# Optimization experiments

Measured on AMD Instinct MI355X. Metric: run time of the kernel, lower is better.

The kernel has to match this reference:

```python
import jax, jax.numpy as jnp
import numpy as np

N, E, F, H, G, C = 50000, 800000, 768, 256, 512, 2  # H = nhid*2 (nhid=128), G graphs, C classes
NHID = 128


def setup_inputs() -> dict:
    key = jax.random.key(0)
    ks = jax.random.split(key, 18)
    s = 0.05
    x = jax.random.normal(ks[0], (N, F), jnp.float32)
    edge_index = jax.random.randint(ks[1], (2, E), 0, N, dtype=jnp.int32)
    # sorted batch vector; every graph non-empty so the 'first node per graph' gather is valid
    batch = ((jnp.arange(N) * G) // N).astype(jnp.int32)
    return {
        "x": x,
        "edge_index": edge_index,
        "batch": batch,
        # GATConv 1 (in=F, out=H, heads=1)
        "W1": jax.random.normal(ks[2], (F, H), jnp.float32) * s,
        "as1": jax.random.normal(ks[3], (H,), jnp.float32) * s,
        "ad1": jax.random.normal(ks[4], (H,), jnp.float32) * s,
        "b1": jnp.zeros((H,), jnp.float32),
        # GATConv 2 (in=H, out=H)
        "W2": jax.random.normal(ks[5], (H, H), jnp.float32) * s,
        "as2": jax.random.normal(ks[6], (H,), jnp.float32) * s,
        "ad2": jax.random.normal(ks[7], (H,), jnp.float32) * s,
        "b2": jnp.zeros((H,), jnp.float32),
        # fc0: num_features -> nhid (news branch)
        "W0": jax.random.normal(ks[8], (F, NHID), jnp.float32) * s,
        "b0": jnp.zeros((NHID,), jnp.float32),
        # fc1: 2*nhid -> nhid (used twice, as in the source)
        "Wf1": jax.random.normal(ks[9], (H, NHID), jnp.float32) * s,
        "bf1": jnp.zeros((NHID,), jnp.float32),
        # fc2: nhid -> num_classes
        "Wf2": jax.random.normal(ks[10], (NHID, C), jnp.float32) * s,
        "bf2": jnp.zeros((C,), jnp.float32),
    }


def _gat(x, src, dst, W, a_s, a_d, b):
    # PyG GATConv, heads=1, concat=True, negative_slope=0.2, self-loops pre-appended to src/dst.
    h = x @ W                                   # [N, H]
    e = jax.nn.leaky_relu((h @ a_s)[src] + (h @ a_d)[dst], 0.2)  # [E+N]
    m = jax.ops.segment_max(e, dst, num_segments=N)
    ex = jnp.exp(e - m[dst])                    # stable segment softmax numerator
    denom = jax.ops.segment_sum(ex, dst, num_segments=N)
    agg = jax.ops.segment_sum(ex[:, None] * h[src], dst, num_segments=N)  # [N, H]
    return agg / denom[:, None] + b


def reference(x, edge_index, batch, W1, as1, ad1, b1, W2, as2, ad2, b2, W0, b0, Wf1, bf1, Wf2, bf2):
    loop = jnp.arange(N, dtype=edge_index.dtype)
    src = jnp.concatenate([edge_index[0], loop])  # add self-loops (PyG default)
    dst = jnp.concatenate([edge_index[1], loop])
    h = jax.nn.selu(_gat(x, src, dst, W1, as1, ad1, b1))
    h = jax.nn.selu(_gat(h, src, dst, W2, as2, ad2, b2))
    # global mean pool over graphs
    cnt = jax.ops.segment_sum(jnp.ones((N,), h.dtype), batch, num_segments=G)
    pooled = jax.nn.selu(jax.ops.segment_sum(h, batch, num_segments=G) / cnt[:, None])
    z = jax.nn.selu(pooled @ Wf1 + bf1)
    # dropout(p=0.5) in eval mode -> identity
    # concat branch: first node of each graph (news root)
    first_idx = jax.ops.segment_min(jnp.arange(N), batch, num_segments=G)
    news = jax.nn.relu(x[first_idx] @ W0 + b0)
    z = jnp.concatenate([z, news], axis=1)       # [G, 2*nhid]
    z = jax.nn.relu(z @ Wf1 + bf1)
    return jax.nn.log_softmax(z @ Wf2 + bf2, axis=-1)
```

## Files before the change

kernel.cpp:

```cpp
#include <hip/hip_runtime.h>
#include <hip/hip_bf16.h>
#include <cstdint>
#include <cstddef>

#define NN 50000
#define EE 800000
#define FF 768
#define HH 256
#define GG 512
#define CC 2
#define NHIDD 128
#define ETOT (EE + NN)
#define NCHUNK 49

typedef __attribute__((ext_vector_type(8))) short bf16x8;
typedef __attribute__((ext_vector_type(4))) float f32x4;
typedef __attribute__((ext_vector_type(8))) unsigned short us8;

__device__ __forceinline__ float b2f(unsigned short u){
  union { float f; uint32_t i; } v; v.i = ((uint32_t)u) << 16; return v.f;
}
__device__ __forceinline__ unsigned short f2b(float f){
  uint32_t u = __float_as_uint(f);
  uint32_t r = (u + 0x7fffu + ((u >> 16) & 1u)) >> 16;
  return (unsigned short)r;
}
__device__ __forceinline__ uint32_t cvtpk(float a, float b){
  uint32_t d;
  asm volatile("v_cvt_pk_bf16_f32 %0, %1, %2" : "=v"(d) : "v"(a), "v"(b));
  return d;
}
__device__ __forceinline__ float selu_f(float x){
  const float lam = 1.0507009873554805f, alp = 1.6732632423543772f;
  return x > 0.f ? lam * x : lam * alp * (__expf(x) - 1.f);
}

__device__ __forceinline__ void gload_lds16(const void* g, void* l){
  __builtin_amdgcn_global_load_lds((const __attribute__((address_space(1))) void*)g,
                                   (__attribute__((address_space(3))) void*)l, 16, 0, 0);
}

__global__ __launch_bounds__(256) void swizzleW2(const float* __restrict__ W1, const float* __restrict__ W2,
                                                 unsigned short* __restrict__ Wsw1, unsigned short* __restrict__ Wsw2){
  int i = blockIdx.x * 256 + threadIdx.x;
  if (i < FF * HH){
    int k = i / HH, n = i % HH;
    Wsw1[(size_t)(k >> 5) * 8192 + n * 32 + (k & 31)] = f2b(W1[i]);
  } else {
    int i2 = i - FF * HH;
    int k = i2 / HH, n = i2 % HH;
    Wsw2[(size_t)(k >> 5) * 8192 + n * 32 + (k & 31)] = f2b(W2[i2]);
  }
}

__global__ __launch_bounds__(256) void zero_deg(int* deg){
  int i = blockIdx.x * 256 + threadIdx.x;
  if (i < NN) deg[i] = 0;
}

__global__ __launch_bounds__(256) void deg_kernel(const int* __restrict__ dstA, int* __restrict__ deg){
  int i = blockIdx.x * 256 + threadIdx.x;
  if (i < ETOT){
    int d = (i < EE) ? dstA[i] : (i - EE);
    atomicAdd(&deg[d], 1);
  }
}

__global__ __launch_bounds__(256) void scanA(const int* __restrict__ deg, int* __restrict__ bsum){
  __shared__ int red[256];
  int c = blockIdx.x, tid = threadIdx.x;
  int base = c * 1024 + tid * 4;
  int s = 0;
#pragma unroll
  for (int j = 0; j < 4; j++){ int idx = base + j; if (idx < NN) s += deg[idx]; }
  red[tid] = s; __syncthreads();
  for (int off = 128; off > 0; off >>= 1){
    if (tid < off) red[tid] += red[tid + off];
    __syncthreads();
  }
  if (tid == 0) bsum[c] = red[0];
}

__global__ __launch_bounds__(256) void scanC(const int* __restrict__ deg, const int* __restrict__ bsum,
                                             int* __restrict__ row_ptr, int* __restrict__ fill_ptr){
  __shared__ int ts[256];
  __shared__ int cbase;
  int c = blockIdx.x, tid = threadIdx.x;
  int pb = (tid < c) ? bsum[tid] : 0;
  ts[tid] = pb; __syncthreads();
  for (int off = 128; off > 0; off >>= 1){
    if (tid < off) ts[tid] += ts[tid + off];
    __syncthreads();
  }
  if (tid == 0) cbase = ts[0];
  __syncthreads();
  int base = c * 1024 + tid * 4;
  int v[4]; int s = 0;
#pragma unroll
  for (int j = 0; j < 4; j++){ int idx = base + j; v[j] = (idx < NN) ? deg[idx] : 0; s += v[j]; }
  ts[tid] = s; __syncthreads();
  for (int off = 1; off < 256; off <<= 1){
    int add = (tid >= off) ? ts[tid - off] : 0;
    __syncthreads();
    ts[tid] += add;
    __syncthreads();
  }
  int run = ts[tid] - s + cbase;
#pragma unroll
  for (int j = 0; j < 4; j++){
    int idx = base + j;
    if (idx < NN){ row_ptr[idx] = run; fill_ptr[idx] = run; }
    run += v[j];
  }
  if (c == 0 && tid == 0) row_ptr[NN] = ETOT;
}

__global__ __launch_bounds__(256) void fill_kernel(const int* __restrict__ srcA, const int* __restrict__ dstA,
                                                   int* __restrict__ fill_ptr, int* __restrict__ csr_src){
  int i = blockIdx.x * 256 + threadIdx.x;
  if (i < ETOT){
    int s = (i < EE) ? srcA[i] : (i - EE);
    int d = (i < EE) ? dstA[i] : (i - EE);
    int pos = atomicAdd(&fill_ptr[d], 1);
    csr_src[pos] = s;
  }
}

__global__ __launch_bounds__(256, 3) void gemm1_f32(const float* __restrict__ A,
                                                 const unsigned short* __restrict__ Wsw,
                                                 const float* __restrict__ a_s, const float* __restrict__ a_d,
                                                 unsigned short* __restrict__ out,
                                                 float* __restrict__ als, float* __restrict__ ald, int M){
  __shared__ float Alf[32 * 384];
  const int tid = threadIdx.x;
  const int m0 = blockIdx.x * 32;
  const int lane = tid & 63, w = tid >> 6;
  const int koff = (lane >> 4) * 8;
  const int arow = lane & 15;
  const int nrow = w * 64 + (lane & 15);

  f32x4 acc[2][4];
#pragma unroll
  for (int rt = 0; rt < 2; rt++)
#pragma unroll
    for (int ct = 0; ct < 4; ct++) acc[rt][ct] = (f32x4){0.f, 0.f, 0.f, 0.f};

  const unsigned short* bbase = Wsw + ((size_t)nrow * 32 + koff);
  bf16x8 bcur[2][4];

  auto stage_half = [&](int p){
#pragma unroll
    for (int j = 0; j < 12; j++){
      int L16 = j * 256 + tid;
      int row = L16 / 96;
      int ch  = L16 - row * 96;
      int sch = ch ^ (row & 7);
      int gr  = m0 + row; if (gr >= M) gr = M - 1;
      gload_lds16(A + (size_t)gr * FF + p * 384 + sch * 4,
                  Alf + (size_t)(j * 256 + w * 64) * 4);
    }
  };

#pragma unroll
  for (int p = 0; p < 2; p++){
    if (p == 1) __syncthreads();
    stage_half(p);
#pragma unroll
    for (int k2 = 0; k2 < 2; k2++)
#pragma unroll
      for (int ct = 0; ct < 4; ct++)
        bcur[k2][ct] = *(const bf16x8*)(bbase + (size_t)(p * 12 + k2) * 8192 + ct * 512);
    __syncthreads();

    for (int ks = 0; ks < 6; ks++){
      bf16x8 bnext[2][4];
      if (ks + 1 < 6){
#pragma unroll
        for (int k2 = 0; k2 < 2; k2++)
#pragma unroll
          for (int ct = 0; ct < 4; ct++)
            bnext[k2][ct] = *(const bf16x8*)(bbase + (size_t)(p * 12 + (ks + 1) * 2 + k2) * 8192 + ct * 512);
      }
      bf16x8 af[2][2];
#pragma unroll
      for (int k2 = 0; k2 < 2; k2++)
#pragma unroll
        for (int rt = 0; rt < 2; rt++){
          int R = rt * 16 + arow;
          int c = ks * 16 + k2 * 8 + (lane >> 4) * 2;
          int m = R & 7;
          float4 v0 = *(const float4*)&Alf[R * 384 + ((c)     ^ m) * 4];
          float4 v1 = *(const float4*)&Alf[R * 384 + ((c + 1) ^ m) * 4];
          union { bf16x8 v; uint32_t u[4]; } X;
          X.u[0] = cvtpk(v0.x, v0.y); X.u[1] = cvtpk(v0.z, v0.w);
          X.u[2] = cvtpk(v1.x, v1.y); X.u[3] = cvtpk(v1.z, v1.w);
          af[k2][rt] = X.v;
        }
#pragma unroll
      for (int k2 = 0; k2 < 2; k2++)
#pragma unroll
        for (int rt = 0; rt < 2; rt++)
#pragma unroll
          for (int ct = 0; ct < 4; ct++)
            acc[rt][ct] = __builtin_amdgcn_mfma_f32_16x16x32_bf16(af[k2][rt], bcur[k2][ct], acc[rt][ct], 0, 0, 0);
      if (ks + 1 < 6){
#pragma unroll
        for (int k2 = 0; k2 < 2; k2++)
#pragma unroll
          for (int ct = 0; ct < 4; ct++) bcur[k2][ct] = bnext[k2][ct];
      }
    }
  }

#pragma unroll
  for (int rt = 0; rt < 2; rt++){
    int mbase = m0 + rt * 16 + (lane >> 4) * 4;
#pragma unroll
    for (int r = 0; r < 4; r++){
      int m = mbase + r;
      if (m < M){
        size_t ro = (size_t)m * HH + w * 64 + (lane & 15);
        out[ro + 0]  = f2b(acc[rt][0][r]);
        out[ro + 16] = f2b(acc[rt][1][r]);
        out[ro + 32] = f2b(acc[rt][2][r]);
        out[ro + 48] = f2b(acc[rt][3][r]);
      }
    }
  }

  float as_c[4], ad_c[4];
#pragma unroll
  for (int ct = 0; ct < 4; ct++){
    int col = w * 64 + ct * 16 + (lane & 15);
    as_c[ct] = a_s[col]; ad_c[ct] = a_d[col];
  }
  float ps[2][4], pd[2][4];
#pragma unroll
  for (int rt = 0; rt < 2; rt++)
#pragma unroll
    for (int r = 0; r < 4; r++){
      float s = 0.f, d = 0.f;
#pragma unroll
      for (int ct = 0; ct < 4; ct++){ float v = acc[rt][ct][r]; s += v * as_c[ct]; d += v * ad_c[ct]; }
      ps[rt][r] = s; pd[rt][r] = d;
    }
#pragma unroll
  for (int off = 1; off < 16; off <<= 1){
#pragma unroll
    for (int rt = 0; rt < 2; rt++)
#pragma unroll
      for (int r = 0; r < 4; r++){
        ps[rt][r] += __shfl_xor(ps[rt][r], off);
        pd[rt][r] += __shfl_xor(pd[rt][r], off);
      }
  }
  __syncthreads();
  float* red = Alf;
  if ((lane & 15) == 0){
    int q = lane >> 4;
#pragma unroll
    for (int rt = 0; rt < 2; rt++)
#pragma unroll
      for (int r = 0; r < 4; r++){
        int row = rt * 16 + q * 4 + r;
        red[w * 32 + row]       = ps[rt][r];
        red[128 + w * 32 + row] = pd[rt][r];
      }
  }
  __syncthreads();
  if (tid < 32){
    float s = red[tid] + red[32 + tid] + red[64 + tid] + red[96 + tid];
    float d = red[128 + tid] + red[160 + tid] + red[192 + tid] + red[224 + tid];
    int m = m0 + tid;
    if (m < M){ als[m] = s; ald[m] = d; }
  }
}

template<int K, int MINW>
__global__ __launch_bounds__(256, MINW) void gemm_mfma(const unsigned short* __restrict__ A,
                                                 const unsigned short* __restrict__ Wsw,
                                                 const float* __restrict__ a_s, const float* __restrict__ a_d,
                                                 unsigned short* __restrict__ out,
                                                 float* __restrict__ als, float* __restrict__ ald, int M){
  constexpr int CHROW = K / 8;
  __shared__ unsigned short Al[32 * K];
  const int tid = threadIdx.x;
  const int m0 = blockIdx.x * 32;
  const int lane = tid & 63, w = tid >> 6;
  const int koff = (lane >> 4) * 8;
  const int arow = lane & 15;
  const int nrow = w * 64 + (lane & 15);

  f32x4 acc[2][4];
#pragma unroll
  for (int rt = 0; rt < 2; rt++)
#pragma unroll
    for (int ct = 0; ct < 4; ct++) acc[rt][ct] = (f32x4){0.f, 0.f, 0.f, 0.f};

  constexpr int ROUNDS = (32 * CHROW) / 256;
#pragma unroll
  for (int j = 0; j < ROUNDS; j++){
    int L16 = j * 256 + tid;
    int row = L16 / CHROW;
    int ch  = L16 - row * CHROW;
    int sch = ch ^ (row & 7);
    int gr  = m0 + row; if (gr >= M) gr = M - 1;
    gload_lds16(A + (size_t)gr * K + sch * 8,
                &Al[(size_t)(j * 256 + w * 64) * 8]);
  }

  const unsigned short* bbase = Wsw + ((size_t)nrow * 32 + koff);
  bf16x8 bcur[2][4];
#pragma unroll
  for (int k2 = 0; k2 < 2; k2++)
#pragma unroll
    for (int ct = 0; ct < 4; ct++)
      bcur[k2][ct] = *(const bf16x8*)(bbase + (size_t)k2 * 8192 + ct * 512);

  __syncthreads();

  constexpr int NIT = K / 64;
  for (int ks = 0; ks < NIT; ks++){
    bf16x8 bnext[2][4];
    if (ks + 1 < NIT){
#pragma unroll
      for (int k2 = 0; k2 < 2; k2++)
#pragma unroll
        for (int ct = 0; ct < 4; ct++)
          bnext[k2][ct] = *(const bf16x8*)(bbase + (size_t)((ks + 1) * 2 + k2) * 8192 + ct * 512);
    }
    bf16x8 af[2][2];
#pragma unroll
    for (int k2 = 0; k2 < 2; k2++)
#pragma unroll
      for (int rt = 0; rt < 2; rt++){
        int R = rt * 16 + arow;
        int chb = (ks * 8 + k2 * 4 + (lane >> 4)) ^ (R & 7);
        af[k2][rt] = *(const bf16x8*)&Al[(size_t)R * K + chb * 8];
      }
#pragma unroll
    for (int k2 = 0; k2 < 2; k2++)
#pragma unroll
      for (int rt = 0; rt < 2; rt++)
#pragma unroll
        for (int ct = 0; ct < 4; ct++)
          acc[rt][ct] = __builtin_amdgcn_mfma_f32_16x16x32_bf16(af[k2][rt], bcur[k2][ct], acc[rt][ct], 0, 0, 0);
    if (ks + 1 < NIT){
#pragma unroll
      for (int k2 = 0; k2 < 2; k2++)
#pragma unroll
        for (int ct = 0; ct < 4; ct++) bcur[k2][ct] = bnext[k2][ct];
    }
  }

#pragma unroll
  for (int rt = 0; rt < 2; rt++){
    int mbase = m0 + rt * 16 + (lane >> 4) * 4;
#pragma unroll
    for (int r = 0; r < 4; r++){
      int m = mbase + r;
      if (m < M){
        size_t ro = (size_t)m * HH + w * 64 + (lane & 15);
        out[ro + 0]  = f2b(acc[rt][0][r]);
        out[ro + 16] = f2b(acc[rt][1][r]);
        out[ro + 32] = f2b(acc[rt][2][r]);
        out[ro + 48] = f2b(acc[rt][3][r]);
      }
    }
  }

  float as_c[4], ad_c[4];
#pragma unroll
  for (int ct = 0; ct < 4; ct++){
    int col = w * 64 + ct * 16 + (lane & 15);
    as_c[ct] = a_s[col]; ad_c[ct] = a_d[col];
  }
  float ps[2][4], pd[2][4];
#pragma unroll
  for (int rt = 0; rt < 2; rt++)
#pragma unroll
    for (int r = 0; r < 4; r++){
      float s = 0.f, d = 0.f;
#pragma unroll
      for (int ct = 0; ct < 4; ct++){ float v = acc[rt][ct][r]; s += v * as_c[ct]; d += v * ad_c[ct]; }
      ps[rt][r] = s; pd[rt][r] = d;
    }
#pragma unroll
  for (int off = 1; off < 16; off <<= 1){
#pragma unroll
    for (int rt = 0; rt < 2; rt++)
#pragma unroll
      for (int r = 0; r < 4; r++){
        ps[rt][r] += __shfl_xor(ps[rt][r], off);
        pd[rt][r] += __shfl_xor(pd[rt][r], off);
      }
  }
  __syncthreads();
  float* red = (float*)Al;
  if ((lane & 15) == 0){
    int q = lane >> 4;
#pragma unroll
    for (int rt = 0; rt < 2; rt++)
#pragma unroll
      for (int r = 0; r < 4; r++){
        int row = rt * 16 + q * 4 + r;
        red[w * 32 + row]       = ps[rt][r];
        red[128 + w * 32 + row] = pd[rt][r];
      }
  }
  __syncthreads();
  if (tid < 32){
    float s = red[tid] + red[32 + tid] + red[64 + tid] + red[96 + tid];
    float d = red[128 + tid] + red[160 + tid] + red[192 + tid] + red[224 + tid];
    int m = m0 + tid;
    if (m < M){ als[m] = s; ald[m] = d; }
  }
}

__global__ __launch_bounds__(256) void agg_wave(const unsigned short* __restrict__ h,
    const float* __restrict__ als, const float* __restrict__ ald,
    const int* __restrict__ row_ptr, const int* __restrict__ csr_src,
    const float* __restrict__ bias, unsigned short* __restrict__ outp){
  int node = blockIdx.x * 4 + (threadIdx.x >> 6);
  int lane = threadIdx.x & 63;
  if (node >= NN) return;
  int base = row_ptr[node];
  int deg  = row_ptr[node + 1] - base;
  float aldd = ald[node];
  float den = 0.f;
  float a[8] = {0.f, 0.f, 0.f, 0.f, 0.f, 0.f, 0.f, 0.f};
  const int f8 = (lane & 31) * 8;
  const int half = lane >> 5;
  for (int p0 = 0; p0 < deg; p0 += 64){
    int cnt = min(64, deg - p0);
    float ev = 0.f; int s = 0;
    if (lane < cnt){
      s = csr_src[base + p0 + lane];
      float v = als[s] + aldd;
      v = v > 0.f ? v : 0.2f * v;
      ev = __expf(v);
    }
    den += ev;
    int j = 0;
    for (; j + 8 <= cnt; j += 8){
      int j0 = j + half, j1 = j + 2 + half, j2 = j + 4 + half, j3 = j + 6 + half;
      int s0 = __shfl(s, j0), s1 = __shfl(s, j1), s2 = __shfl(s, j2), s3 = __shfl(s, j3);
      float e0 = __shfl(ev, j0), e1 = __shfl(ev, j1), e2 = __shfl(ev, j2), e3 = __shfl(ev, j3);
      us8 g0 = *(const us8*)&h[(size_t)s0 * HH + f8];
      us8 g1 = *(const us8*)&h[(size_t)s1 * HH + f8];
      us8 g2 = *(const us8*)&h[(size_t)s2 * HH + f8];
      us8 g3 = *(const us8*)&h[(size_t)s3 * HH + f8];
#pragma unroll
      for (int i = 0; i < 8; i++) a[i] += e0 * b2f(g0[i]) + e1 * b2f(g1[i]);
#pragma unroll
      for (int i = 0; i < 8; i++) a[i] += e2 * b2f(g2[i]) + e3 * b2f(g3[i]);
    }
    for (; j + 4 <= cnt; j += 4){
      int j0 = j + half, j1 = j + 2 + half;
      int s0 = __shfl(s, j0), s1 = __shfl(s, j1);
      float e0 = __shfl(ev, j0), e1 = __shfl(ev, j1);
      us8 g0 = *(const us8*)&h[(size_t)s0 * HH + f8];
      us8 g1 = *(const us8*)&h[(size_t)s1 * HH + f8];
#pragma unroll
      for (int i = 0; i < 8; i++) a[i] += e0 * b2f(g0[i]) + e1 * b2f(g1[i]);
    }
    for (; j < cnt; j += 2){
      int jj = j + half;
      int sj = __shfl(s, jj & 63);
      float ejr = __shfl(ev, jj & 63);
      float ej = (jj < cnt) ? ejr : 0.f;
      us8 gj = *(const us8*)&h[(size_t)sj * HH + f8];
#pragma unroll
      for (int i = 0; i < 8; i++) a[i] += ej * b2f(gj[i]);
    }
  }
  for (int off = 32; off > 0; off >>= 1) den += __shfl_xor(den, off);
#pragma unroll
  for (int i = 0; i < 8; i++) a[i] += __shfl_xor(a[i], 32);
  if (lane < 32){
    float inv = 1.f / den;
    float4 b4a = *(const float4*)&bias[f8];
    float4 b4b = *(const float4*)&bias[f8 + 4];
    us8 o;
    o[0] = f2b(selu_f(a[0] * inv + b4a.x));
    o[1] = f2b(selu_f(a[1] * inv + b4a.y));
    o[2] = f2b(selu_f(a[2] * inv + b4a.z));
    o[3] = f2b(selu_f(a[3] * inv + b4a.w));
    o[4] = f2b(selu_f(a[4] * inv + b4b.x));
    o[5] = f2b(selu_f(a[5] * inv + b4b.y));
    o[6] = f2b(selu_f(a[6] * inv + b4b.z));
    o[7] = f2b(selu_f(a[7] * inv + b4b.w));
    *(us8*)&outp[(size_t)node * HH + f8] = o;
  }
}

__global__ __launch_bounds__(256) void head_kernel(const unsigned short* __restrict__ x3,
    const int* __restrict__ batch, const float* __restrict__ x,
    const float* __restrict__ W0, const float* __restrict__ b0,
    const float* __restrict__ Wf1, const float* __restrict__ bf1,
    const float* __restrict__ Wf2, const float* __restrict__ bf2,
    float* __restrict__ out){
  __shared__ float pr[HH];
  __shared__ float xr[FF];
  __shared__ float zc[HH];
  __shared__ int se[2];
  __shared__ float l0s[2], l1s[2];
  int g = blockIdx.x, t = threadIdx.x;
  if (t < 2){
    int target = g + t, lo = 0, hi = NN;
    while (lo < hi){ int mid = (lo + hi) >> 1; if (batch[mid] < target) lo = mid + 1; else hi = mid; }
    se[t] = lo;
  }
  __syncthreads();
  int s = se[0], e = se[1];
  {
    float acc = 0.f;
    for (int n = s; n < e; n++) acc += b2f(x3[(size_t)n * HH + t]);
    pr[t] = selu_f(acc / (float)(e - s));
  }
  for (int k = t; k < FF; k += 256) xr[k] = x[(size_t)s * FF + k];
  __syncthreads();
  if (t < NHIDD){
    float acc = 0.f;
    for (int k = 0; k < HH; k++) acc += pr[k] * Wf1[k * NHIDD + t];
    zc[t] = selu_f(acc + bf1[t]);
  } else {
    int t2 = t - NHIDD;
    float acc = 0.f;
    for (int k = 0; k < FF; k++) acc += xr[k] * W0[k * NHIDD + t2];
    acc += b0[t2];
    zc[NHIDD + t2] = acc > 0.f ? acc : 0.f;
  }
  __syncthreads();
  if (t < NHIDD){
    float acc = 0.f;
    for (int k = 0; k < HH; k++) acc += zc[k] * Wf1[k * NHIDD + t];
    float z2 = acc + bf1[t]; z2 = z2 > 0.f ? z2 : 0.f;
    float p0 = z2 * Wf2[t * CC + 0];
    float p1 = z2 * Wf2[t * CC + 1];
    for (int off = 32; off > 0; off >>= 1){ p0 += __shfl_xor(p0, off); p1 += __shfl_xor(p1, off); }
    if ((t & 63) == 0){ l0s[t >> 6] = p0; l1s[t >> 6] = p1; }
  }
  __syncthreads();
  if (t == 0){
    float l0 = l0s[0] + l0s[1] + bf2[0];
    float l1 = l1s[0] + l1s[1] + bf2[1];
    float mx = fmaxf(l0, l1);
    float lse = mx + logf(__expf(l0 - mx) + __expf(l1 - mx));
    out[g * CC + 0] = l0 - lse;
    out[g * CC + 1] = l1 - lse;
  }
}

extern "C" void kernel_launch(void* const* d_in, const int* in_sizes, int n_in,
                              void* d_out, int out_size, void* d_ws, size_t ws_size,
                              hipStream_t stream){
  const float* x          = (const float*)d_in[0];
  const int* edge_index   = (const int*)d_in[1];
  const int* batch        = (const int*)d_in[2];
  const float* W1  = (const float*)d_in[3];
  const float* as1 = (const float*)d_in[4];
  const float* ad1 = (const float*)d_in[5];
  const float* b1  = (const float*)d_in[6];
  const float* W2  = (const float*)d_in[7];
  const float* as2 = (const float*)d_in[8];
  const float* ad2 = (const float*)d_in[9];
  const float* b2  = (const float*)d_in[10];
  const float* W0  = (const float*)d_in[11];
  const float* b0  = (const float*)d_in[12];
  const float* Wf1 = (const float*)d_in[13];
  const float* bf1 = (const float*)d_in[14];
  const float* Wf2 = (const float*)d_in[15];
  const float* bf2 = (const float*)d_in[16];
  float* out = (float*)d_out;

  char* w = (char*)d_ws;
  size_t off = 0;
  auto alloc = [&](size_t bytes){ size_t o = off; off += (bytes + 255) & ~(size_t)255; return o; };
  unsigned short* h    = (unsigned short*)(w + alloc((size_t)NN * HH * 2));
  unsigned short* x2   = (unsigned short*)(w + alloc((size_t)NN * HH * 2));
  unsigned short* Wsw1 = (unsigned short*)(w + alloc((size_t)FF * HH * 2));
  unsigned short* Wsw2 = (unsigned short*)(w + alloc((size_t)HH * HH * 2));
  float* als     = (float*)(w + alloc((size_t)NN * 4));
  float* ald     = (float*)(w + alloc((size_t)NN * 4));
  int*   deg     = (int*)(w + alloc((size_t)NN * 4));
  int*   row_ptr = (int*)(w + alloc((size_t)(NN + 1) * 4));
  int*   fillp   = (int*)(w + alloc((size_t)NN * 4));
  int*   csr_src = (int*)(w + alloc((size_t)ETOT * 4));
  int*   bsum    = (int*)(w + alloc(64 * 4));

  const int* srcA = edge_index;
  const int* dstA = edge_index + EE;

  swizzleW2<<<(FF * HH + HH * HH) / 256, 256, 0, stream>>>(W1, W2, Wsw1, Wsw2);

  zero_deg<<<(NN + 255) / 256, 256, 0, stream>>>(deg);
  deg_kernel<<<(ETOT + 255) / 256, 256, 0, stream>>>(dstA, deg);
  scanA<<<NCHUNK, 256, 0, stream>>>(deg, bsum);
  scanC<<<NCHUNK, 256, 0, stream>>>(deg, bsum, row_ptr, fillp);
  fill_kernel<<<(ETOT + 255) / 256, 256, 0, stream>>>(srcA, dstA, fillp, csr_src);

  const int gemm_grid = (NN + 31) / 32;
  gemm1_f32<<<gemm_grid, 256, 0, stream>>>(x, Wsw1, as1, ad1, h, als, ald, NN);
  agg_wave<<<(NN + 3) / 4, 256, 0, stream>>>(h, als, ald, row_ptr, csr_src, b1, x2);
  gemm_mfma<HH, 3><<<gemm_grid, 256, 0, stream>>>(x2, Wsw2, as2, ad2, h, als, ald, NN);
  agg_wave<<<(NN + 3) / 4, 256, 0, stream>>>(h, als, ald, row_ptr, csr_src, b2, x2);
  head_kernel<<<GG, 256, 0, stream>>>(x2, batch, x, W0, b0, Wf1, bf1, Wf2, bf2, out);
}
```

Baseline: 580.5 us.

## Software-pipeline aggregation gathers, pin GEMM prefetch registers, memset degree buffer

```diff
diff --git a/kernel.cpp b/kernel.cpp
--- a/kernel.cpp
+++ b/kernel.cpp
@@ -33,6 +33,17 @@
 __device__ __forceinline__ float selu_f(float x){
   const float lam = 1.0507009873554805f, alp = 1.6732632423543772f;
   return x > 0.f ? lam * x : lam * alp * (__expf(x) - 1.f);
+}
+
+__device__ __forceinline__ void keepalive(bf16x8& v){
+  union { bf16x8 v; uint32_t u[4]; } t; t.v = v;
+  asm volatile("" : "+v"(t.u[0]), "+v"(t.u[1]), "+v"(t.u[2]), "+v"(t.u[3]));
+  v = t.v;
+}
+__device__ __forceinline__ void keepalive(us8& v){
+  union { us8 v; uint32_t u[4]; } t; t.v = v;
+  asm volatile("" : "+v"(t.u[0]), "+v"(t.u[1]), "+v"(t.u[2]), "+v"(t.u[3]));
+  v = t.v;
 }
 
 __device__ __forceinline__ void gload_lds16(const void* g, void* l){
@@ -53,11 +64,6 @@
   }
 }
 
-__global__ __launch_bounds__(256) void zero_deg(int* deg){
-  int i = blockIdx.x * 256 + threadIdx.x;
-  if (i < NN) deg[i] = 0;
-}
-
 __global__ __launch_bounds__(256) void deg_kernel(const int* __restrict__ dstA, int* __restrict__ deg){
   int i = blockIdx.x * 256 + threadIdx.x;
   if (i < ETOT){
@@ -126,7 +132,7 @@
   }
 }
 
-__global__ __launch_bounds__(256, 3) void gemm1_f32(const float* __restrict__ A,
+__global__ __launch_bounds__(256, 2) void gemm1_f32(const float* __restrict__ A,
                                                  const unsigned short* __restrict__ Wsw,
                                                  const float* __restrict__ a_s, const float* __restrict__ a_d,
                                                  unsigned short* __restrict__ out,
@@ -168,8 +174,10 @@
 #pragma unroll
     for (int k2 = 0; k2 < 2; k2++)
 #pragma unroll
-      for (int ct = 0; ct < 4; ct++)
+      for (int ct = 0; ct < 4; ct++){
         bcur[k2][ct] = *(const bf16x8*)(bbase + (size_t)(p * 12 + k2) * 8192 + ct * 512);
+        keepalive(bcur[k2][ct]);
+      }
     __syncthreads();
 
     for (int ks = 0; ks < 6; ks++){
@@ -178,8 +186,10 @@
 #pragma unroll
         for (int k2 = 0; k2 < 2; k2++)
 #pragma unroll
-          for (int ct = 0; ct < 4; ct++)
+          for (int ct = 0; ct < 4; ct++){
             bnext[k2][ct] = *(const bf16x8*)(bbase + (size_t)(p * 12 + (ks + 1) * 2 + k2) * 8192 + ct * 512);
+            keepalive(bnext[k2][ct]);
+          }
       }
       bf16x8 af[2][2];
 #pragma unroll
@@ -442,18 +452,37 @@
     }
     den += ev;
     int j = 0;
-    for (; j + 8 <= cnt; j += 8){
+    us8 ga[4]; float ea[4];
+    if (j + 8 <= cnt){
       int j0 = j + half, j1 = j + 2 + half, j2 = j + 4 + half, j3 = j + 6 + half;
       int s0 = __shfl(s, j0), s1 = __shfl(s, j1), s2 = __shfl(s, j2), s3 = __shfl(s, j3);
-      float e0 = __shfl(ev, j0), e1 = __shfl(ev, j1), e2 = __shfl(ev, j2), e3 = __shfl(ev, j3);
-      us8 g0 = *(const us8*)&h[(size_t)s0 * HH + f8];
-      us8 g1 = *(const us8*)&h[(size_t)s1 * HH + f8];
-      us8 g2 = *(const us8*)&h[(size_t)s2 * HH + f8];
-      us8 g3 = *(const us8*)&h[(size_t)s3 * HH + f8];
-#pragma unroll
-      for (int i = 0; i < 8; i++) a[i] += e0 * b2f(g0[i]) + e1 * b2f(g1[i]);
-#pragma unroll
-      for (int i = 0; i < 8; i++) a[i] += e2 * b2f(g2[i]) + e3 * b2f(g3[i]);
+      ea[0] = __shfl(ev, j0); ea[1] = __shfl(ev, j1); ea[2] = __shfl(ev, j2); ea[3] = __shfl(ev, j3);
+      ga[0] = *(const us8*)&h[(size_t)s0 * HH + f8]; keepalive(ga[0]);
+      ga[1] = *(const us8*)&h[(size_t)s1 * HH + f8]; keepalive(ga[1]);
+      ga[2] = *(const us8*)&h[(size_t)s2 * HH + f8]; keepalive(ga[2]);
+      ga[3] = *(const us8*)&h[(size_t)s3 * HH + f8]; keepalive(ga[3]);
+    }
+    for (; j + 8 <= cnt; j += 8){
+      us8 gb[4]; float eb[4];
+      bool more = (j + 16 <= cnt);
+      if (more){
+        int jn = j + 8;
+        int j0 = jn + half, j1 = jn + 2 + half, j2 = jn + 4 + half, j3 = jn + 6 + half;
+        int s0 = __shfl(s, j0), s1 = __shfl(s, j1), s2 = __shfl(s, j2), s3 = __shfl(s, j3);
+        eb[0] = __shfl(ev, j0); eb[1] = __shfl(ev, j1); eb[2] = __shfl(ev, j2); eb[3] = __shfl(ev, j3);
+        gb[0] = *(const us8*)&h[(size_t)s0 * HH + f8]; keepalive(gb[0]);
+        gb[1] = *(const us8*)&h[(size_t)s1 * HH + f8]; keepalive(gb[1]);
+        gb[2] = *(const us8*)&h[(size_t)s2 * HH + f8]; keepalive(gb[2]);
+        gb[3] = *(const us8*)&h[(size_t)s3 * HH + f8]; keepalive(gb[3]);
+      }
+#pragma unroll
+      for (int i = 0; i < 8; i++) a[i] += ea[0] * b2f(ga[0][i]) + ea[1] * b2f(ga[1][i]);
+#pragma unroll
+      for (int i = 0; i < 8; i++) a[i] += ea[2] * b2f(ga[2][i]) + ea[3] * b2f(ga[3][i]);
+      if (more){
+#pragma unroll
+        for (int q = 0; q < 4; q++){ ga[q] = gb[q]; ea[q] = eb[q]; }
+      }
     }
     for (; j + 4 <= cnt; j += 4){
       int j0 = j + half, j1 = j + 2 + half;
@@ -594,7 +623,7 @@
 
   swizzleW2<<<(FF * HH + HH * HH) / 256, 256, 0, stream>>>(W1, W2, Wsw1, Wsw2);
 
-  zero_deg<<<(NN + 255) / 256, 256, 0, stream>>>(deg);
+  hipMemsetAsync(deg, 0, (size_t)NN * 4, stream);
   deg_kernel<<<(ETOT + 255) / 256, 256, 0, stream>>>(dstA, deg);
   scanA<<<NCHUNK, 256, 0, stream>>>(deg, bsum);
   scanC<<<NCHUNK, 256, 0, stream>>>(deg, bsum, row_ptr, fillp);
```

Result: slower. 662.8 us (+14.2%).
